# Performance work log

Hardware: AMD Instinct MI355X
Metric: run time of the kernel (lower is better)

Reference implementation:

```python
import jax, jax.numpy as jnp
import numpy as np
import math

B, S, T, D, H = 4, 1024, 1024, 512, 8
EPS = 1e-5

def setup_inputs() -> dict:
    key = jax.random.key(0)
    ks = iter(jax.random.split(key, 40))
    w = lambda *shp: jax.random.normal(next(ks), shp, jnp.float32) * 0.02
    inp = {
        'x': jax.random.normal(next(ks), (B, S, D), jnp.float32),
        'encod_out': jax.random.normal(next(ks), (B, T, D), jnp.float32),
    }
    for p in ('sa', 'ca'):
        inp[p + '_wq'] = w(H, D, D); inp[p + '_bq'] = w(H, D)
        inp[p + '_wk'] = w(H, D, D); inp[p + '_bk'] = w(H, D)
        inp[p + '_wv'] = w(H, D, D); inp[p + '_bv'] = w(H, D)
        inp[p + '_wo'] = w(H, D, D); inp[p + '_bo'] = w(H, D)
        inp[p + '_wf'] = w(H * D, D); inp[p + '_bf'] = w(D)
    for i in (1, 2, 3):
        inp[f'ln{i}_g'] = jnp.ones((D,), jnp.float32)
        inp[f'ln{i}_b'] = jnp.zeros((D,), jnp.float32)
    inp['fc1_w'] = w(D, 4 * D); inp['fc1_b'] = w(4 * D)
    inp['fc2_w'] = w(4 * D, D); inp['fc2_b'] = w(D)
    return inp

def _ln(x, g, b):
    m = jnp.mean(x, -1, keepdims=True)
    v = jnp.mean((x - m) ** 2, -1, keepdims=True)
    return (x - m) / jnp.sqrt(v + EPS) * g + b

def _mha(xq, xkv, wq, bq, wk, bk, wv, bv, wo, bo, wf, bf, mask):
    # per-head FULL-width projections, stacked on head axis h
    Q = jnp.einsum('bsd,hdf->bhsf', xq, wq) + bq[None, :, None, :]
    K = jnp.einsum('btd,hdf->bhtf', xkv, wk) + bk[None, :, None, :]
    V = jnp.einsum('btd,hdf->bhtf', xkv, wv) + bv[None, :, None, :]
    scores = jnp.einsum('bhsf,bhtf->bhst', Q, K) / math.sqrt(Q.shape[-1])
    if mask is not None:
        scores = jnp.where(mask == 0, -jnp.inf, scores)
    A = jax.nn.softmax(scores, axis=-1)
    O = jnp.einsum('bhst,bhtf->bhsf', A, V)
    O = jnp.einsum('bhsf,hfg->bhsg', O, wo) + bo[None, :, None, :]  # per-head out_linear
    cat = O.transpose(0, 2, 1, 3).reshape(O.shape[0], O.shape[2], -1)  # [B,S,H*D]
    return cat @ wf + bf

def reference(x, encod_out,
              sa_wq, sa_bq, sa_wk, sa_bk, sa_wv, sa_bv, sa_wo, sa_bo, sa_wf, sa_bf,
              ca_wq, ca_bq, ca_wk, ca_bk, ca_wv, ca_bv, ca_wo, ca_bo, ca_wf, ca_bf,
              ln1_g, ln1_b, ln2_g, ln2_b, ln3_g, ln3_b,
              fc1_w, fc1_b, fc2_w, fc2_b):
    s = x.shape[1]
    mask = jnp.tril(jnp.ones((s, s), x.dtype))
    h = _mha(x, x, sa_wq, sa_bq, sa_wk, sa_bk, sa_wv, sa_bv, sa_wo, sa_bo, sa_wf, sa_bf, mask)
    x1 = _ln(h + x, ln1_g, ln1_b)
    h = _mha(x1, encod_out, ca_wq, ca_bq, ca_wk, ca_bk, ca_wv, ca_bv, ca_wo, ca_bo, ca_wf, ca_bf, None)
    x2 = _ln(h + x1, ln2_g, ln2_b)
    ff = jax.nn.relu(x2 @ fc1_w + fc1_b) @ fc2_w + fc2_b
    return _ln(ff + x2, ln3_g, ln3_b)
```

## Files before the change

### kernel.cpp

```cpp
#include <hip/hip_runtime.h>
#include <hip/hip_bf16.h>

typedef __hip_bfloat16 bf16;
typedef __attribute__((ext_vector_type(8))) __bf16 bf16x8;
typedef __attribute__((ext_vector_type(4))) float f32x4;

typedef const __attribute__((address_space(1))) void cg_void;
typedef __attribute__((address_space(3))) void lds_void;

__device__ inline float b2f(bf16 v) { return __bfloat162float(v); }
__device__ inline bf16 f2b(float v) { return __float2bfloat16(v); }
__device__ inline float ldf(const float* p) { return *p; }
__device__ inline float ldf(const bf16* p) { return __bfloat162float(*p); }

#define BKK 32

template<int BN_, bool BIAS, bool RELU, bool OUT_BF16>
__global__ __launch_bounds__(256) void gemm_bt(
    const bf16* __restrict__ A, const bf16* __restrict__ Bt, void* __restrict__ Cout,
    const float* __restrict__ bias,
    int M, int N, int K, int lda, int ldb, int ldc,
    long aHi, long aLo, long bHi, long bLo, long cHi, long cLo, int zdiv)
{
  alignas(16) __shared__ bf16 As[128 * BKK];
  alignas(16) __shared__ bf16 Bs[BN_ * BKK];
  const int t = threadIdx.x;
  const int l = t & 63;
  const int w = t >> 6;
  const int z = blockIdx.z;
  const int zq = z / zdiv, zr = z % zdiv;
  A += (long)zq * aHi + (long)zr * aLo;
  Bt += (long)zq * bHi + (long)zr * bLo;
  const long cbase = (long)zq * cHi + (long)zr * cLo;
  const int m0 = blockIdx.x * 128;
  const int n0 = blockIdx.y * BN_;

  constexpr int NJ = BN_ / 32;
  f32x4 acc[4][NJ] = {};

  const int r0 = t >> 2;
  const int kc = (t & 3) * 8;
  const bf16* aP0 = A + (long)(m0 + r0) * lda + kc;
  const bf16* aP1 = aP0 + (long)64 * lda;
  bf16* aD0 = As + t * 8;
  bf16* aD1 = As + (t + 256) * 8;
  const bf16* bP0 = Bt + (long)(n0 + r0) * ldb + kc;
  bf16* bD0 = Bs + t * 8;
  const bf16* bP1 = bP0 + (long)64 * ldb;
  bf16* bD1 = Bs + (t + 256) * 8;

  const int fr = l & 15;
  const int fk = (l >> 4) * 8;
  const int aRow = (w >> 1) * 64 + fr;
  const int bRow = (w & 1) * (BN_ / 2) + fr;

  for (int kt = 0; kt < K; kt += BKK) {
    __builtin_amdgcn_global_load_lds((cg_void*)(aP0 + kt), (lds_void*)aD0, 16, 0, 0);
    __builtin_amdgcn_global_load_lds((cg_void*)(aP1 + kt), (lds_void*)aD1, 16, 0, 0);
    __builtin_amdgcn_global_load_lds((cg_void*)(bP0 + kt), (lds_void*)bD0, 16, 0, 0);
    if constexpr (BN_ == 128)
      __builtin_amdgcn_global_load_lds((cg_void*)(bP1 + kt), (lds_void*)bD1, 16, 0, 0);
    __syncthreads();
    bf16x8 af[4], bv[NJ];
#pragma unroll
    for (int i = 0; i < 4; ++i)
      af[i] = *(const bf16x8*)(As + (aRow + i * 16) * BKK + fk);
#pragma unroll
    for (int j = 0; j < NJ; ++j)
      bv[j] = *(const bf16x8*)(Bs + (bRow + j * 16) * BKK + fk);
#pragma unroll
    for (int i = 0; i < 4; ++i)
#pragma unroll
      for (int j = 0; j < NJ; ++j)
        acc[i][j] = __builtin_amdgcn_mfma_f32_16x16x32_bf16(af[i], bv[j], acc[i][j], 0, 0, 0);
    __syncthreads();
  }

  float* cf = (float*)Cout;
  bf16* cb = (bf16*)Cout;
#pragma unroll
  for (int i = 0; i < 4; ++i) {
    const int mb = m0 + (w >> 1) * 64 + i * 16 + ((l >> 4) << 2);
#pragma unroll
    for (int j = 0; j < NJ; ++j) {
      const int nc = n0 + (w & 1) * (BN_ / 2) + j * 16 + fr;
      const float bvv = BIAS ? bias[nc] : 0.f;
#pragma unroll
      for (int r = 0; r < 4; ++r) {
        const int m = mb + r;
        const long off = cbase + (long)m * ldc + nc;
        float vv = acc[i][j][r] + bvv;
        if (RELU) vv = fmaxf(vv, 0.f);
        if (OUT_BF16) cb[off] = f2b(vv);
        else cf[off] = vv;
      }
    }
  }
}

template<int BN_, bool B_, bool R_, bool O_>
static inline void gemmL(hipStream_t st, int M, int N, int K,
                         const bf16* A, int lda, long aHi, long aLo,
                         const bf16* Bt, int ldb, long bHi, long bLo,
                         void* C, int ldc, long cHi, long cLo,
                         int zdiv, int nz, const float* bias)
{
  dim3 g(M / 128, N / BN_, nz);
  gemm_bt<BN_, B_, R_, O_><<<g, dim3(256), 0, st>>>(
      A, Bt, C, bias, M, N, K, lda, ldb, ldc, aHi, aLo, bHi, bLo, cHi, cLo, zdiv);
}

template<typename ST>
__global__ __launch_bounds__(256) void transpose_to_bf16(
    const ST* __restrict__ in, bf16* __restrict__ out, int R, int C, long sIn, long sOut)
{
  __shared__ bf16 tile[32][33];
  const int z = blockIdx.z;
  in += (long)z * sIn;
  out += (long)z * sOut;
  const int tx = threadIdx.x & 31, ty = threadIdx.x >> 5;
  const int c0 = blockIdx.x * 32, r0 = blockIdx.y * 32;
#pragma unroll
  for (int i = 0; i < 4; ++i)
    tile[ty + i * 8][tx] = f2b(ldf(in + (long)(r0 + ty + i * 8) * C + c0 + tx));
  __syncthreads();
#pragma unroll
  for (int i = 0; i < 4; ++i)
    out[(long)(c0 + ty + i * 8) * R + r0 + tx] = tile[tx][ty + i * 8];
}

__global__ __launch_bounds__(256) void cast4_k(
    const float* __restrict__ in, bf16* __restrict__ out, long n4)
{
  long i = (long)blockIdx.x * 256 + threadIdx.x;
  const long st = (long)gridDim.x * 256;
  for (; i < n4; i += st) {
    const float4 v = ((const float4*)in)[i];
    bf16* o = out + i * 4;
    o[0] = f2b(v.x); o[1] = f2b(v.y); o[2] = f2b(v.z); o[3] = f2b(v.w);
  }
}

__global__ __launch_bounds__(256) void fill_sentinel(float* __restrict__ out, long n)
{
  long i = (long)blockIdx.x * 256 + threadIdx.x;
  const long st = (long)gridDim.x * 256;
  for (; i < n; i += st) out[i] = 1.0e6f;
}

__global__ __launch_bounds__(256) void softmax_rows(
    bf16* __restrict__ S, const float* __restrict__ v, float scale, int causal)
{
  const int r = blockIdx.x * 4 + (threadIdx.x >> 6);
  const int l = threadIdx.x & 63;
  const int zl = r >> 10, s = r & 1023;
  bf16* row = S + (long)r * 1024;
  const float* vp = v + (zl >> 2) * 4096 + (zl & 3) * 1024;
  const int t0 = l * 16;
  bf16x8* rp = (bf16x8*)(row + t0);
  const bf16x8 a0 = rp[0], a1 = rp[1];
  float xx[16];
#pragma unroll
  for (int j = 0; j < 8; ++j) { xx[j] = (float)a0[j]; xx[8 + j] = (float)a1[j]; }
  float mx = -3.4e38f;
#pragma unroll
  for (int k = 0; k < 16; ++k) {
    const int tt = t0 + k;
    float val = (xx[k] + vp[tt]) * scale;
    if (causal && tt > s) val = -3.4e38f;
    xx[k] = val;
    mx = fmaxf(mx, val);
  }
#pragma unroll
  for (int d = 1; d < 64; d <<= 1) mx = fmaxf(mx, __shfl_xor(mx, d));
  float sum = 0.f;
#pragma unroll
  for (int k = 0; k < 16; ++k) {
    const float e = (xx[k] > -1e37f) ? __expf(xx[k] - mx) : 0.f;
    xx[k] = e;
    sum += e;
  }
#pragma unroll
  for (int d = 1; d < 64; d <<= 1) sum += __shfl_xor(sum, d);
  const float inv = 1.f / sum;
  bf16x8 r0v, r1v;
#pragma unroll
  for (int j = 0; j < 8; ++j) {
    r0v[j] = (__bf16)(xx[j] * inv);
    r1v[j] = (__bf16)(xx[8 + j] * inv);
  }
  rp[0] = r0v;
  rp[1] = r1v;
}

__global__ __launch_bounds__(256) void ln_fused(
    const float* __restrict__ parts, long zstride, int nz,
    const float* __restrict__ beff, const float* __restrict__ resF,
    const bf16* __restrict__ resB, const float* __restrict__ g,
    const float* __restrict__ b, bf16* __restrict__ outB, float* __restrict__ outF)
{
  const int m = blockIdx.x * 4 + (threadIdx.x >> 6);
  const int l = threadIdx.x & 63;
  float vv[8];
  float s = 0.f;
#pragma unroll
  for (int i = 0; i < 8; ++i) {
    const int c = i * 64 + l;
    float acc = beff[c];
    if (resF) acc += resF[(long)m * 512 + c];
    else acc += b2f(resB[(long)m * 512 + c]);
    for (int zz = 0; zz < nz; ++zz) acc += parts[zz * zstride + (long)m * 512 + c];
    vv[i] = acc;
    s += acc;
  }
#pragma unroll
  for (int d = 1; d < 64; d <<= 1) s += __shfl_xor(s, d);
  const float mean = s * (1.f / 512.f);
  float vs = 0.f;
#pragma unroll
  for (int i = 0; i < 8; ++i) { const float dv = vv[i] - mean; vs += dv * dv; }
#pragma unroll
  for (int d = 1; d < 64; d <<= 1) vs += __shfl_xor(vs, d);
  const float rstd = rsqrtf(vs * (1.f / 512.f) + 1e-5f);
#pragma unroll
  for (int i = 0; i < 8; ++i) {
    const int c = i * 64 + l;
    const float y = (vv[i] - mean) * rstd * g[c] + b[c];
    if (outB) outB[(long)m * 512 + c] = f2b(y);
    if (outF) outF[(long)m * 512 + c] = y;
  }
}

__global__ void beff_init_k(const float* __restrict__ bf_, float* __restrict__ beff)
{
  const int e = blockIdx.x * 256 + threadIdx.x;
  if (e < 512) beff[e] = bf_[e];
}

__global__ __launch_bounds__(256) void beff_wf_k(
    const float* __restrict__ bo, const float* __restrict__ wf, float* __restrict__ beff)
{
  const int t = threadIdx.x;
  const int r0 = blockIdx.x * 128;
  float s0 = 0.f, s1 = 0.f;
  for (int r = 0; r < 128; ++r) {
    const float bb = bo[r0 + r];
    const float* row = wf + (long)(r0 + r) * 512;
    s0 += bb * row[t];
    s1 += bb * row[t + 256];
  }
  atomicAdd(&beff[t], s0);
  atomicAdd(&beff[t + 256], s1);
}

__global__ __launch_bounds__(256) void beff_w2_k(
    const float* __restrict__ bv, const bf16* __restrict__ W2t, float* __restrict__ beff)
{
  const int e = blockIdx.x * 4 + (threadIdx.x >> 6);
  const int l = threadIdx.x & 63;
  const bf16* row = W2t + (long)e * 4096;
  float s = 0.f;
#pragma unroll
  for (int j = 0; j < 8; ++j) {
    const int hf = j * 512 + l * 8;
    const bf16x8 wv = *(const bf16x8*)(row + hf);
    const float4 b0 = *(const float4*)(bv + hf);
    const float4 b1 = *(const float4*)(bv + hf + 4);
    s += (float)wv[0] * b0.x + (float)wv[1] * b0.y + (float)wv[2] * b0.z + (float)wv[3] * b0.w;
    s += (float)wv[4] * b1.x + (float)wv[5] * b1.y + (float)wv[6] * b1.z + (float)wv[7] * b1.w;
  }
#pragma unroll
  for (int d = 1; d < 64; d <<= 1) s += __shfl_xor(s, d);
  if (l == 0) atomicAdd(&beff[e], s);
}

__global__ __launch_bounds__(256) void wkbq_k(
    const float* __restrict__ wk, const float* __restrict__ bq, float* __restrict__ o)
{
  const int id = blockIdx.x * 4 + (threadIdx.x >> 6);
  const int l = threadIdx.x & 63;
  const int h = id >> 9, d = id & 511;
  const float* wp = wk + (long)h * 262144 + (long)d * 512 + l * 8;
  const float* bp = bq + h * 512 + l * 8;
  float s = 0.f;
#pragma unroll
  for (int j = 0; j < 2; ++j) {
    const float4 a = *(const float4*)(wp + j * 4);
    const float4 b = *(const float4*)(bp + j * 4);
    s += a.x * b.x + a.y * b.y + a.z * b.z + a.w * b.w;
  }
#pragma unroll
  for (int dd = 1; dd < 64; dd <<= 1) s += __shfl_xor(s, dd);
  if (l == 0) o[id] = s;
}

__global__ __launch_bounds__(256) void rank1_v(
    const bf16* __restrict__ kvB, const float* __restrict__ wkbq, float* __restrict__ v)
{
  const int m = blockIdx.x * 4 + (threadIdx.x >> 6);
  const int l = threadIdx.x & 63;
  const bf16x8 row = *(const bf16x8*)(kvB + (long)m * 512 + l * 8);
  float rf[8];
#pragma unroll
  for (int j = 0; j < 8; ++j) rf[j] = (float)row[j];
  for (int h = 0; h < 8; ++h) {
    const float* wp = wkbq + h * 512 + l * 8;
    float p = 0.f;
#pragma unroll
    for (int j = 0; j < 8; ++j) p += rf[j] * wp[j];
#pragma unroll
    for (int d = 1; d < 64; d <<= 1) p += __shfl_xor(p, d);
    if (l == 0) v[(long)h * 4096 + m] = p;
  }
}

extern "C" void kernel_launch(void* const* d_in, const int* in_sizes, int n_in,
                              void* d_out, int out_size, void* d_ws, size_t ws_size,
                              hipStream_t stream)
{
  (void)in_sizes; (void)n_in;
  const float* x = (const float*)d_in[0];
  const float* enc = (const float*)d_in[1];
  const float* ln_g[3] = {(const float*)d_in[22], (const float*)d_in[24], (const float*)d_in[26]};
  const float* ln_b[3] = {(const float*)d_in[23], (const float*)d_in[25], (const float*)d_in[27]};
  const float* fc1_w = (const float*)d_in[28];
  const float* fc1_b = (const float*)d_in[29];
  const float* fc2_w = (const float*)d_in[30];
  const float* fc2_b = (const float*)d_in[31];

  const float scale = 0.044194173824159216f;
  char* base = (char*)d_ws;
  const long MB = 1024 * 1024;

  bf16* Xb    = (bf16*)(base + 0 * MB);
  bf16* Eb    = (bf16*)(base + 4 * MB);
  bf16* x1b   = (bf16*)(base + 8 * MB);
  bf16* x2b   = (bf16*)(base + 12 * MB);
  bf16* fc1T  = (bf16*)(base + 16 * MB);
  bf16* fc2T  = (bf16*)(base + 18 * MB);
  float* vbuf = (float*)(base + 20 * MB);
  float* wkbq = (float*)(base + 20 * MB + 256 * 1024);
  float* beff = (float*)(base + 20 * MB + 512 * 1024);
  bf16* XT    = (bf16*)(base + 21 * MB);
  bf16* WqkT  = (bf16*)(base + 25 * MB);
  bf16* W3cat = (bf16*)(base + 29 * MB);
  char* Treg  = base + 33 * MB;
  char* screg = base + 65 * MB;
  char* axreg = base + 81 * MB;

  bf16* T      = (bf16*)Treg;
  float* parts = (float*)Treg;
  bf16* scores = (bf16*)screg;
  bf16* W2t    = (bf16*)screg;
  bf16* wfT    = (bf16*)(screg + 4 * MB);
  bf16* AX     = (bf16*)axreg;
  bf16* wqB    = (bf16*)axreg;
  bf16* wkB    = (bf16*)(axreg + 4 * MB);
  bf16* wvB    = (bf16*)(axreg + 8 * MB);
  bf16* woB    = (bf16*)(axreg + 12 * MB);
  bf16* Hb     = (bf16*)axreg;

  if (ws_size < (size_t)(113 * MB)) {
    fill_sentinel<<<dim3(2048), dim3(256), 0, stream>>>((float*)d_out, (long)out_size);
    return;
  }

  cast4_k<<<dim3(512), dim3(256), 0, stream>>>(x, Xb, 4096L * 512 / 4);
  cast4_k<<<dim3(512), dim3(256), 0, stream>>>(enc, Eb, 4096L * 512 / 4);
  transpose_to_bf16<float><<<dim3(64, 16, 1), dim3(256), 0, stream>>>(fc1_w, fc1T, 512, 2048, 0, 0);
  transpose_to_bf16<float><<<dim3(16, 64, 1), dim3(256), 0, stream>>>(fc2_w, fc2T, 2048, 512, 0, 0);

  auto run_attn = [&](int ib, const bf16* qB, const bf16* kvB,
                      const float* resF, const bf16* resB, int causal,
                      const float* lg, const float* lb, bf16* outB) {
    const float* wq = (const float*)d_in[ib + 0];
    const float* bq = (const float*)d_in[ib + 1];
    const float* wk = (const float*)d_in[ib + 2];
    const float* wv = (const float*)d_in[ib + 4];
    const float* bv = (const float*)d_in[ib + 5];
    const float* wo = (const float*)d_in[ib + 6];
    const float* bo = (const float*)d_in[ib + 7];
    const float* wf = (const float*)d_in[ib + 8];
    const float* bfv = (const float*)d_in[ib + 9];

    cast4_k<<<dim3(512), dim3(256), 0, stream>>>(wq, wqB, 2097152 / 4);
    cast4_k<<<dim3(512), dim3(256), 0, stream>>>(wk, wkB, 2097152 / 4);
    cast4_k<<<dim3(512), dim3(256), 0, stream>>>(wv, wvB, 2097152 / 4);
    cast4_k<<<dim3(512), dim3(256), 0, stream>>>(wo, woB, 2097152 / 4);
    transpose_to_bf16<float><<<dim3(16, 128, 1), dim3(256), 0, stream>>>(wf, wfT, 4096, 512, 0, 0);
    gemmL<64, false, false, true>(stream, 512, 512, 512,
        wfT, 4096, 512, 0, woB, 512, 262144, 0, W2t, 4096, 512, 0, 1, 8, nullptr);
    beff_init_k<<<dim3(2), dim3(256), 0, stream>>>(bfv, beff);
    beff_wf_k<<<dim3(32), dim3(256), 0, stream>>>(bo, wf, beff);
    beff_w2_k<<<dim3(128), dim3(256), 0, stream>>>(bv, W2t, beff);
    gemmL<64, false, false, true>(stream, 512, 512, 512,
        wkB, 512, 262144, 0, wqB, 512, 262144, 0, WqkT, 512, 262144, 0, 1, 8, nullptr);
    gemmL<64, false, false, true>(stream, 512, 512, 512,
        W2t, 4096, 512, 0, wvB, 512, 262144, 0, W3cat, 4096, 512, 0, 1, 8, nullptr);
    wkbq_k<<<dim3(1024), dim3(256), 0, stream>>>(wk, bq, wkbq);
    rank1_v<<<dim3(1024), dim3(256), 0, stream>>>(kvB, wkbq, vbuf);
    transpose_to_bf16<bf16><<<dim3(16, 32, 4), dim3(256), 0, stream>>>(
        kvB, XT, 1024, 512, 524288, 524288);
    gemmL<128, false, false, true>(stream, 4096, 4096, 512,
        qB, 512, 0, 0, WqkT, 512, 0, 0, T, 4096, 0, 0, 1, 1, nullptr);

    for (int c = 0; c < 4; ++c) {
      gemmL<128, false, false, true>(stream, 1024, 1024, 512,
          T + 2 * c * 512, 4096, 512, 4194304,
          kvB, 512, 0, 524288,
          scores, 1024, 4194304, 1048576, 4, 8, nullptr);
      softmax_rows<<<dim3(2048), dim3(256), 0, stream>>>(
          scores, vbuf + 2 * c * 4096, scale, causal);
      gemmL<64, false, false, true>(stream, 1024, 512, 1024,
          scores, 1024, 4194304, 1048576,
          XT, 1024, 0, 524288,
          AX + 2 * c * 512, 4096, 512, 4194304, 4, 8, nullptr);
    }
    gemmL<64, false, false, false>(stream, 4096, 512, 1024,
        AX, 4096, 1024, 0, W3cat, 4096, 1024, 0,
        parts, 512, 2097152, 0, 1, 4, nullptr);
    ln_fused<<<dim3(1024), dim3(256), 0, stream>>>(
        parts, 2097152, 4, beff, resF, resB, lg, lb, outB, nullptr);
  };

  run_attn(2, Xb, Xb, x, nullptr, 1, ln_g[0], ln_b[0], x1b);
  run_attn(12, x1b, Eb, nullptr, x1b, 0, ln_g[1], ln_b[1], x2b);

  gemmL<128, true, true, true>(stream, 4096, 2048, 512,
      x2b, 512, 0, 0, fc1T, 512, 0, 0, Hb, 2048, 0, 0, 1, 1, fc1_b);
  gemmL<64, false, false, false>(stream, 4096, 512, 512,
      Hb, 2048, 512, 0, fc2T, 2048, 512, 0, parts, 512, 2097152, 0, 1, 4, nullptr);
  ln_fused<<<dim3(1024), dim3(256), 0, stream>>>(
      parts, 2097152, 4, fc2_b, nullptr, x2b, ln_g[2], ln_b[2], nullptr, (float*)d_out);
}
```

Measured before the change: 947.7 us.

## Batch attention over all heads, swizzle GEMM block order, fuse weight casts

The per-chunk loop over head pairs is replaced with single batched score, softmax and AV launches covering all 8 heads. This needs a larger workspace, so the buffers are no longer aliased and the size check rises to 193 MB. The GEMM kernel now remaps block indices across 8 groups, likely to spread concurrently running tiles across XCDs or caches. The four weight casts are merged into one launch. The intent is to cut launch count and fill the GPU better, at the cost of more workspace memory and traffic for the full scores buffer.

```diff
diff --git a/kernel.cpp b/kernel.cpp
--- a/kernel.cpp
+++ b/kernel.cpp
@@ -32,8 +32,14 @@
   A += (long)zq * aHi + (long)zr * aLo;
   Bt += (long)zq * bHi + (long)zr * bLo;
   const long cbase = (long)zq * cHi + (long)zr * cLo;
-  const int m0 = blockIdx.x * 128;
-  const int n0 = blockIdx.y * BN_;
+
+  const int gx = gridDim.x;
+  int bid = blockIdx.y * gx + blockIdx.x;
+  const int nwg = gx * gridDim.y;
+  if ((nwg & 7) == 0)
+    bid = (bid & 7) * (nwg >> 3) + (bid >> 3);
+  const int m0 = (bid % gx) * 128;
+  const int n0 = (bid / gx) * BN_;
 
   constexpr int NJ = BN_ / 32;
   f32x4 acc[4][NJ] = {};
@@ -132,6 +138,28 @@
 __global__ __launch_bounds__(256) void cast4_k(
     const float* __restrict__ in, bf16* __restrict__ out, long n4)
 {
+  long i = (long)blockIdx.x * 256 + threadIdx.x;
+  const long st = (long)gridDim.x * 256;
+  for (; i < n4; i += st) {
+    const float4 v = ((const float4*)in)[i];
+    bf16* o = out + i * 4;
+    o[0] = f2b(v.x); o[1] = f2b(v.y); o[2] = f2b(v.z); o[3] = f2b(v.w);
+  }
+}
+
+__global__ __launch_bounds__(256) void cast4x4_k(
+    const float* __restrict__ p0, const float* __restrict__ p1,
+    const float* __restrict__ p2, const float* __restrict__ p3,
+    bf16* __restrict__ o0, bf16* __restrict__ o1,
+    bf16* __restrict__ o2, bf16* __restrict__ o3, long n4)
+{
+  const float* in; bf16* out;
+  switch (blockIdx.y) {
+    case 0: in = p0; out = o0; break;
+    case 1: in = p1; out = o1; break;
+    case 2: in = p2; out = o2; break;
+    default: in = p3; out = o3; break;
+  }
   long i = (long)blockIdx.x * 256 + threadIdx.x;
   const long st = (long)gridDim.x * 256;
   for (; i < n4; i += st) {
@@ -344,23 +372,19 @@
   bf16* XT    = (bf16*)(base + 21 * MB);
   bf16* WqkT  = (bf16*)(base + 25 * MB);
   bf16* W3cat = (bf16*)(base + 29 * MB);
-  char* Treg  = base + 33 * MB;
-  char* screg = base + 65 * MB;
-  char* axreg = base + 81 * MB;
-
-  bf16* T      = (bf16*)Treg;
-  float* parts = (float*)Treg;
-  bf16* scores = (bf16*)screg;
-  bf16* W2t    = (bf16*)screg;
-  bf16* wfT    = (bf16*)(screg + 4 * MB);
-  bf16* AX     = (bf16*)axreg;
-  bf16* wqB    = (bf16*)axreg;
-  bf16* wkB    = (bf16*)(axreg + 4 * MB);
-  bf16* wvB    = (bf16*)(axreg + 8 * MB);
-  bf16* woB    = (bf16*)(axreg + 12 * MB);
-  bf16* Hb     = (bf16*)axreg;
-
-  if (ws_size < (size_t)(113 * MB)) {
+  bf16* T     = (bf16*)(base + 33 * MB);
+  float* parts = (float*)(base + 65 * MB);
+  bf16* scores = (bf16*)(base + 97 * MB);
+  bf16* AX    = (bf16*)(base + 161 * MB);
+  bf16* wqB   = (bf16*)(base + 97 * MB);
+  bf16* wkB   = (bf16*)(base + 101 * MB);
+  bf16* wvB   = (bf16*)(base + 105 * MB);
+  bf16* woB   = (bf16*)(base + 109 * MB);
+  bf16* wfT   = (bf16*)(base + 113 * MB);
+  bf16* W2t   = (bf16*)(base + 117 * MB);
+  bf16* Hb    = (bf16*)(base + 97 * MB);
+
+  if (ws_size < (size_t)(193 * MB)) {
     fill_sentinel<<<dim3(2048), dim3(256), 0, stream>>>((float*)d_out, (long)out_size);
     return;
   }
@@ -383,10 +407,8 @@
     const float* wf = (const float*)d_in[ib + 8];
     const float* bfv = (const float*)d_in[ib + 9];
 
-    cast4_k<<<dim3(512), dim3(256), 0, stream>>>(wq, wqB, 2097152 / 4);
-    cast4_k<<<dim3(512), dim3(256), 0, stream>>>(wk, wkB, 2097152 / 4);
-    cast4_k<<<dim3(512), dim3(256), 0, stream>>>(wv, wvB, 2097152 / 4);
-    cast4_k<<<dim3(512), dim3(256), 0, stream>>>(wo, woB, 2097152 / 4);
+    cast4x4_k<<<dim3(512, 4), dim3(256), 0, stream>>>(
+        wq, wk, wv, wo, wqB, wkB, wvB, woB, 2097152 / 4);
     transpose_to_bf16<float><<<dim3(16, 128, 1), dim3(256), 0, stream>>>(wf, wfT, 4096, 512, 0, 0);
     gemmL<64, false, false, true>(stream, 512, 512, 512,
         wfT, 4096, 512, 0, woB, 512, 262144, 0, W2t, 4096, 512, 0, 1, 8, nullptr);
@@ -404,18 +426,15 @@
     gemmL<128, false, false, true>(stream, 4096, 4096, 512,
         qB, 512, 0, 0, WqkT, 512, 0, 0, T, 4096, 0, 0, 1, 1, nullptr);
 
-    for (int c = 0; c < 4; ++c) {
-      gemmL<128, false, false, true>(stream, 1024, 1024, 512,
-          T + 2 * c * 512, 4096, 512, 4194304,
-          kvB, 512, 0, 524288,
-          scores, 1024, 4194304, 1048576, 4, 8, nullptr);
-      softmax_rows<<<dim3(2048), dim3(256), 0, stream>>>(
-          scores, vbuf + 2 * c * 4096, scale, causal);
-      gemmL<64, false, false, true>(stream, 1024, 512, 1024,
-          scores, 1024, 4194304, 1048576,
-          XT, 1024, 0, 524288,
-          AX + 2 * c * 512, 4096, 512, 4194304, 4, 8, nullptr);
-    }
+    gemmL<128, false, false, true>(stream, 1024, 1024, 512,
+        T, 4096, 512, 4194304,
+        kvB, 512, 0, 524288,
+        scores, 1024, 4194304, 1048576, 4, 32, nullptr);
+    softmax_rows<<<dim3(8192), dim3(256), 0, stream>>>(scores, vbuf, scale, causal);
+    gemmL<64, false, false, true>(stream, 1024, 512, 1024,
+        scores, 1024, 4194304, 1048576,
+        XT, 1024, 0, 524288,
+        AX, 4096, 512, 4194304, 4, 32, nullptr);
     gemmL<64, false, false, false>(stream, 4096, 512, 1024,
         AX, 4096, 1024, 0, W3cat, 4096, 1024, 0,
         parts, 512, 2097152, 0, 1, 4, nullptr);
```

Result: no change. 959.2 us (+1.2%).
